# Kernel tuning notes

Measured on AMD Instinct MI355X. Metric: run time of the kernel, lower is better.

## Reference

```python
import jax, jax.numpy as jnp
import numpy as np

NEG_SLOPE = 0.2


def setup_inputs() -> dict:
    key = jax.random.key(0)
    ks = jax.random.split(key, 5)
    N, E, Din, Dout = 100000, 1600000, 64, 64
    x = jax.random.normal(ks[0], (N, Din), dtype=jnp.float32)
    edge_index = jax.random.randint(ks[1], (2, E), 0, N, dtype=jnp.int64)
    # Glorot-ish scale for weights
    W_l = jax.random.normal(ks[2], (Din, Dout), dtype=jnp.float32) / np.sqrt(Din)
    W_r = jax.random.normal(ks[3], (Din, Dout), dtype=jnp.float32) / np.sqrt(Din)
    att = jax.random.normal(ks[4], (Dout,), dtype=jnp.float32) / np.sqrt(Dout)
    bias = jnp.zeros((Dout,), dtype=jnp.float32)
    return {"x": x, "edge_index": edge_index, "W_l": W_l, "W_r": W_r, "att": att, "bias": bias}


def reference(x, edge_index, W_l, W_r, att, bias):
    N = x.shape[0]
    # PyG GATv2Conv default: add self loops
    loop = jnp.arange(N, dtype=edge_index.dtype)
    src = jnp.concatenate([edge_index[0], loop])  # j (source / message)
    dst = jnp.concatenate([edge_index[1], loop])  # i (target / aggregation)

    x_l = x @ W_l  # [N, Dout] source transform
    x_r = x @ W_r  # [N, Dout] target transform

    # per-edge attention logit: att . LeakyReLU(x_l[j] + x_r[i])
    e = jax.nn.leaky_relu(x_l[src] + x_r[dst], NEG_SLOPE) @ att  # [E+N]

    # segment softmax grouped by destination node
    e_max = jax.ops.segment_max(e, dst, num_segments=N)  # [N]
    e_exp = jnp.exp(e - e_max[dst])
    denom = jax.ops.segment_sum(e_exp, dst, num_segments=N)  # [N]
    alpha = e_exp / denom[dst]  # [E+N]

    # weighted scatter-add aggregation of source features
    out = jax.ops.segment_sum(alpha[:, None] * x_l[src], dst, num_segments=N)
    return out + bias
```

## Files before the change

kernel.cpp:

```cpp
#include <hip/hip_runtime.h>

#define NEG_SLOPE 0.2f
#define CH 8192
#define BW 512
#define CAP2 10240

__global__ __launch_bounds__(256) void k_gemm(const float* __restrict__ x,
                                              const float* __restrict__ Wl,
                                              const float* __restrict__ Wr,
                                              float* __restrict__ xl,
                                              float* __restrict__ xr, int N) {
    __shared__ float sX[128 * 64];
    __shared__ float sW[64 * 128];
    const int t = threadIdx.x;
    const int B = blockIdx.x * 128;

    for (int f = t; f < 2048; f += 256) {
        const int k = f >> 5, cg = f & 31;
        float4 v;
        if (cg < 16) v = reinterpret_cast<const float4*>(Wl)[k * 16 + cg];
        else         v = reinterpret_cast<const float4*>(Wr)[k * 16 + (cg - 16)];
        reinterpret_cast<float4*>(sW)[f] = v;
    }
    for (int f = t; f < 2048; f += 256) {
        const int r = B + (f >> 4);
        float4 v = {0.f, 0.f, 0.f, 0.f};
        if (r < N) v = reinterpret_cast<const float4*>(x)[(size_t)B * 16 + f];
        reinterpret_cast<float4*>(sX)[f] = v;
    }
    __syncthreads();

    const int cg = t & 31;
    const int g  = t >> 5;

    float4 acc[16];
#pragma unroll
    for (int i = 0; i < 16; i++) acc[i] = make_float4(0.f, 0.f, 0.f, 0.f);

    for (int kk = 0; kk < 64; kk += 4) {
        const float4 w0 = reinterpret_cast<const float4*>(sW)[(kk + 0) * 32 + cg];
        const float4 w1 = reinterpret_cast<const float4*>(sW)[(kk + 1) * 32 + cg];
        const float4 w2 = reinterpret_cast<const float4*>(sW)[(kk + 2) * 32 + cg];
        const float4 w3 = reinterpret_cast<const float4*>(sW)[(kk + 3) * 32 + cg];
#pragma unroll
        for (int i = 0; i < 16; i++) {
            const float4 xv = reinterpret_cast<const float4*>(sX)[(g * 16 + i) * 16 + (kk >> 2)];
            acc[i].x = fmaf(xv.x, w0.x, acc[i].x);
            acc[i].y = fmaf(xv.x, w0.y, acc[i].y);
            acc[i].z = fmaf(xv.x, w0.z, acc[i].z);
            acc[i].w = fmaf(xv.x, w0.w, acc[i].w);
            acc[i].x = fmaf(xv.y, w1.x, acc[i].x);
            acc[i].y = fmaf(xv.y, w1.y, acc[i].y);
            acc[i].z = fmaf(xv.y, w1.z, acc[i].z);
            acc[i].w = fmaf(xv.y, w1.w, acc[i].w);
            acc[i].x = fmaf(xv.z, w2.x, acc[i].x);
            acc[i].y = fmaf(xv.z, w2.y, acc[i].y);
            acc[i].z = fmaf(xv.z, w2.z, acc[i].z);
            acc[i].w = fmaf(xv.z, w2.w, acc[i].w);
            acc[i].x = fmaf(xv.w, w3.x, acc[i].x);
            acc[i].y = fmaf(xv.w, w3.y, acc[i].y);
            acc[i].z = fmaf(xv.w, w3.z, acc[i].z);
            acc[i].w = fmaf(xv.w, w3.w, acc[i].w);
        }
    }

    const int c = cg * 4;
    float* dstp = (c < 64) ? (xl + c) : (xr + (c - 64));
#pragma unroll
    for (int i = 0; i < 16; i++) {
        const int r = B + g * 16 + i;
        if (r < N) *reinterpret_cast<float4*>(dstp + (size_t)r * 64) = acc[i];
    }
}

__global__ __launch_bounds__(256) void k_part(const int* __restrict__ src,
                                              const int* __restrict__ dst,
                                              int* __restrict__ bcount,
                                              int* __restrict__ part,
                                              int E, int M, int NB) {
    __shared__ int lhist[512];
    __shared__ int lbase[512];
    const int t = threadIdx.x;
    const int b = blockIdx.x;
    const int lo = b * CH, hi = min(M, lo + CH);

    for (int i = t; i < NB; i += 256) lhist[i] = 0;
    __syncthreads();
    for (int k = lo + t; k < hi; k += 256) {
        const int d = (k < E) ? dst[k] : k - E;
        atomicAdd(&lhist[d >> 9], 1);
    }
    __syncthreads();
    for (int i = t; i < NB; i += 256) {
        const int c = lhist[i];
        lbase[i] = c ? atomicAdd(&bcount[i], c) : 0;
    }
    __syncthreads();
    for (int i = t; i < NB; i += 256) lhist[i] = 0;
    __syncthreads();
    for (int k = lo + t; k < hi; k += 256) {
        int s, d;
        if (k < E) { s = src[k]; d = dst[k]; } else { s = k - E; d = s; }
        const int bkt = d >> 9;
        const int pos = lbase[bkt] + atomicAdd(&lhist[bkt], 1);
        if (pos < CAP2) part[(size_t)bkt * CAP2 + pos] = (s << 9) | (d & 511);
    }
}

__global__ __launch_bounds__(256) void k_bsort(const int* __restrict__ part,
                                               const int* __restrict__ bcount,
                                               int* __restrict__ sedge,
                                               int* __restrict__ off,
                                               int* __restrict__ deg, int N) {
    __shared__ int keys[CAP2];
    __shared__ int lhist[512];
    __shared__ int lcur[512];
    __shared__ int sh2[256];
    const int t = threadIdx.x;
    const int bkt = blockIdx.x;
    const int base = bkt * CAP2;
    const int n = min(bcount[bkt], CAP2);

    for (int i = t; i < 512; i += 256) lhist[i] = 0;
    __syncthreads();
    for (int i = t; i < n; i += 256) {
        const int k = part[base + i];
        keys[i] = k;
        atomicAdd(&lhist[k & 511], 1);
    }
    __syncthreads();

    const int a0 = lhist[2 * t], a1 = lhist[2 * t + 1];
    const int ps = a0 + a1;
    sh2[t] = ps;
    __syncthreads();
    for (int o = 1; o < 256; o <<= 1) {
        int v = (t >= o) ? sh2[t - o] : 0;
        __syncthreads();
        sh2[t] += v;
        __syncthreads();
    }
    const int ex = sh2[t] - ps;
    lcur[2 * t]     = base + ex;
    lcur[2 * t + 1] = base + ex + a0;
    const int d0 = (bkt << 9) + 2 * t;
    if (d0 < N)     { off[d0] = base + ex;          deg[d0] = a0; }
    if (d0 + 1 < N) { off[d0 + 1] = base + ex + a0; deg[d0 + 1] = a1; }
    __syncthreads();

    for (int i = t; i < n; i += 256) {
        const int k = keys[i];
        const int pos = atomicAdd(&lcur[k & 511], 1);
        sedge[pos] = k >> 9;
    }
}

__global__ void k_fused(const int* __restrict__ offv, const int* __restrict__ degv,
                        const int* __restrict__ sedge, const float* __restrict__ xl,
                        const float* __restrict__ xr, const float* __restrict__ att,
                        const float* __restrict__ bias, float* __restrict__ out, int N) {
    const int lane = threadIdx.x & 63;
    const int gl = lane & 15;
    const int q = lane >> 4;
    int wave = (blockIdx.x * blockDim.x + threadIdx.x) >> 6;
    const int nw = (gridDim.x * blockDim.x) >> 6;
    const float4 a = reinterpret_cast<const float4*>(att)[gl];
    const float4 b = reinterpret_cast<const float4*>(bias)[gl];
    for (int i = wave; i < N; i += nw) {
        const int base = offv[i];
        const int dg = degv[i];
        const float4 xri = reinterpret_cast<const float4*>(xr)[(size_t)i * 16 + gl];
        float s = 0.f;
        float4 acc = {0.f, 0.f, 0.f, 0.f};
        for (int t = q; t < dg; t += 4) {
            const int j = sedge[base + t];
            const float4 l = reinterpret_cast<const float4*>(xl)[(size_t)j * 16 + gl];
            float v0 = l.x + xri.x; v0 = fmaxf(v0, NEG_SLOPE * v0);
            float v1 = l.y + xri.y; v1 = fmaxf(v1, NEG_SLOPE * v1);
            float v2 = l.z + xri.z; v2 = fmaxf(v2, NEG_SLOPE * v2);
            float v3 = l.w + xri.w; v3 = fmaxf(v3, NEG_SLOPE * v3);
            float p = a.x * v0 + a.y * v1 + a.z * v2 + a.w * v3;
            p += __shfl_xor(p, 1, 16);
            p += __shfl_xor(p, 2, 16);
            p += __shfl_xor(p, 4, 16);
            p += __shfl_xor(p, 8, 16);
            const float w = __expf(p);
            s += w;
            acc.x = fmaf(w, l.x, acc.x);
            acc.y = fmaf(w, l.y, acc.y);
            acc.z = fmaf(w, l.z, acc.z);
            acc.w = fmaf(w, l.w, acc.w);
        }
        s += __shfl_xor(s, 16); s += __shfl_xor(s, 32);
        acc.x += __shfl_xor(acc.x, 16); acc.x += __shfl_xor(acc.x, 32);
        acc.y += __shfl_xor(acc.y, 16); acc.y += __shfl_xor(acc.y, 32);
        acc.z += __shfl_xor(acc.z, 16); acc.z += __shfl_xor(acc.z, 32);
        acc.w += __shfl_xor(acc.w, 16); acc.w += __shfl_xor(acc.w, 32);
        if (q == 0) {
            const float inv = 1.f / s;
            float4 o;
            o.x = fmaf(acc.x, inv, b.x);
            o.y = fmaf(acc.y, inv, b.y);
            o.z = fmaf(acc.z, inv, b.z);
            o.w = fmaf(acc.w, inv, b.w);
            reinterpret_cast<float4*>(out)[(size_t)i * 16 + gl] = o;
        }
    }
}

extern "C" void kernel_launch(void* const* d_in, const int* in_sizes, int n_in,
                              void* d_out, int out_size, void* d_ws, size_t ws_size,
                              hipStream_t stream) {
    const float* x    = (const float*)d_in[0];
    const int*   ei   = (const int*)d_in[1];
    const float* Wl   = (const float*)d_in[2];
    const float* Wr   = (const float*)d_in[3];
    const float* att  = (const float*)d_in[4];
    const float* bias = (const float*)d_in[5];
    float* out = (float*)d_out;

    const int N = in_sizes[0] / 64;
    const int E = in_sizes[1] / 2;
    const int M = E + N;
    const int ng  = (N + 127) / 128;
    const int nch = (M + CH - 1) / CH;
    const int NB  = (N + BW - 1) / BW;

    float* xl = (float*)d_ws;
    float* xr = xl + (size_t)N * 64;
    int* deg    = (int*)(xr + (size_t)N * 64);
    int* off    = deg + N;
    int* bcount = off + N;
    int* part   = bcount + NB;
    int* sedge  = part + (size_t)NB * CAP2;

    hipMemsetAsync(bcount, 0, (size_t)NB * sizeof(int), stream);

    k_gemm<<<ng, 256, 0, stream>>>(x, Wl, Wr, xl, xr, N);
    k_part<<<nch, 256, 0, stream>>>(ei, ei + E, bcount, part, E, M, NB);
    k_bsort<<<NB, 256, 0, stream>>>(part, bcount, sedge, off, deg, N);
    k_fused<<<2048, 256, 0, stream>>>(off, deg, sedge, xl, xr, att, bias, out, N);
}
```

Baseline: 238.9 us.

## Store projected features in fp16 and coalesce partition and sort scatters via LDS

The projected source and target features are now written and gathered as fp16, which halves the bytes moved by the random per-edge gathers in the fused aggregation kernel. The partition kernel now reads its edges into registers, ranks them per bucket in shared memory, and writes them out bucket-contiguously instead of scattering with per-edge atomics. The bucket sort stages its sorted output in LDS before a coalesced store. fp16 storage loses precision in the attention logits and aggregated features, and the larger shared-memory use in the partition and sort kernels may reduce occupancy.

```diff
diff --git a/kernel.cpp b/kernel.cpp
--- a/kernel.cpp
+++ b/kernel.cpp
@@ -1,15 +1,17 @@
 #include <hip/hip_runtime.h>
+#include <hip/hip_fp16.h>
 
 #define NEG_SLOPE 0.2f
-#define CH 8192
+#define CH 4096
+#define UN 16
 #define BW 512
 #define CAP2 10240
 
 __global__ __launch_bounds__(256) void k_gemm(const float* __restrict__ x,
                                               const float* __restrict__ Wl,
                                               const float* __restrict__ Wr,
-                                              float* __restrict__ xl,
-                                              float* __restrict__ xr, int N) {
+                                              __half* __restrict__ xl,
+                                              __half* __restrict__ xr, int N) {
     __shared__ float sX[128 * 64];
     __shared__ float sW[64 * 128];
     const int t = threadIdx.x;
@@ -65,11 +67,21 @@
     }
 
     const int c = cg * 4;
-    float* dstp = (c < 64) ? (xl + c) : (xr + (c - 64));
+    __half* dstp = (c < 64) ? (xl + c) : (xr + (c - 64));
 #pragma unroll
     for (int i = 0; i < 16; i++) {
         const int r = B + g * 16 + i;
-        if (r < N) *reinterpret_cast<float4*>(dstp + (size_t)r * 64) = acc[i];
+        if (r < N) {
+            __half2 h01, h23;
+            h01.x = __float2half_rn(acc[i].x);
+            h01.y = __float2half_rn(acc[i].y);
+            h23.x = __float2half_rn(acc[i].z);
+            h23.y = __float2half_rn(acc[i].w);
+            uint2 u;
+            u.x = *reinterpret_cast<unsigned int*>(&h01);
+            u.y = *reinterpret_cast<unsigned int*>(&h23);
+            *reinterpret_cast<uint2*>(dstp + (size_t)r * 64) = u;
+        }
     }
 }
 
@@ -78,32 +90,66 @@
                                               int* __restrict__ bcount,
                                               int* __restrict__ part,
                                               int E, int M, int NB) {
-    __shared__ int lhist[512];
-    __shared__ int lbase[512];
+    __shared__ int skey[CH];
+    __shared__ unsigned char sbkt[CH];
+    __shared__ int hist[256];
+    __shared__ int lcur[256];
+    __shared__ int gofs[256];
     const int t = threadIdx.x;
     const int b = blockIdx.x;
-    const int lo = b * CH, hi = min(M, lo + CH);
-
-    for (int i = t; i < NB; i += 256) lhist[i] = 0;
-    __syncthreads();
-    for (int k = lo + t; k < hi; k += 256) {
-        const int d = (k < E) ? dst[k] : k - E;
-        atomicAdd(&lhist[d >> 9], 1);
-    }
-    __syncthreads();
-    for (int i = t; i < NB; i += 256) {
-        const int c = lhist[i];
-        lbase[i] = c ? atomicAdd(&bcount[i], c) : 0;
-    }
-    __syncthreads();
-    for (int i = t; i < NB; i += 256) lhist[i] = 0;
-    __syncthreads();
-    for (int k = lo + t; k < hi; k += 256) {
-        int s, d;
-        if (k < E) { s = src[k]; d = dst[k]; } else { s = k - E; d = s; }
-        const int bkt = d >> 9;
-        const int pos = lbase[bkt] + atomicAdd(&lhist[bkt], 1);
-        if (pos < CAP2) part[(size_t)bkt * CAP2 + pos] = (s << 9) | (d & 511);
+    const int lo = b * CH;
+    const int cnt = min(M - lo, CH);
+
+    hist[t] = 0;
+    __syncthreads();
+
+    int rs[UN], rd[UN];
+#pragma unroll
+    for (int u = 0; u < UN; u++) {
+        const int k = lo + t + u * 256;
+        rd[u] = -1; rs[u] = 0;
+        if (k < M) {
+            if (k < E) { rs[u] = src[k]; rd[u] = dst[k]; }
+            else       { rs[u] = k - E;  rd[u] = rs[u]; }
+        }
+    }
+#pragma unroll
+    for (int u = 0; u < UN; u++)
+        if (rd[u] >= 0) atomicAdd(&hist[rd[u] >> 9], 1);
+    __syncthreads();
+
+    const int h = hist[t];
+    lcur[t] = h;
+    __syncthreads();
+    for (int o = 1; o < 256; o <<= 1) {
+        const int v = (t >= o) ? lcur[t - o] : 0;
+        __syncthreads();
+        lcur[t] += v;
+        __syncthreads();
+    }
+    const int ex = lcur[t] - h;
+    int gbase = 0;
+    if (t < NB && h > 0) gbase = atomicAdd(&bcount[t], h);
+    __syncthreads();
+    lcur[t] = ex;
+    gofs[t] = t * CAP2 + gbase - ex;
+    __syncthreads();
+
+#pragma unroll
+    for (int u = 0; u < UN; u++) {
+        if (rd[u] >= 0) {
+            const int bkt = rd[u] >> 9;
+            const int p = atomicAdd(&lcur[bkt], 1);
+            skey[p] = (rs[u] << 9) | (rd[u] & 511);
+            sbkt[p] = (unsigned char)bkt;
+        }
+    }
+    __syncthreads();
+
+    for (int i = t; i < cnt; i += 256) {
+        const int bkt = sbkt[i];
+        const int pos = gofs[bkt] + i;
+        if (pos - bkt * CAP2 < CAP2) part[pos] = skey[i];
     }
 }
 
@@ -113,6 +159,7 @@
                                                int* __restrict__ off,
                                                int* __restrict__ deg, int N) {
     __shared__ int keys[CAP2];
+    __shared__ int outk[CAP2];
     __shared__ int lhist[512];
     __shared__ int lcur[512];
     __shared__ int sh2[256];
@@ -141,8 +188,8 @@
         __syncthreads();
     }
     const int ex = sh2[t] - ps;
-    lcur[2 * t]     = base + ex;
-    lcur[2 * t + 1] = base + ex + a0;
+    lcur[2 * t]     = ex;
+    lcur[2 * t + 1] = ex + a0;
     const int d0 = (bkt << 9) + 2 * t;
     if (d0 < N)     { off[d0] = base + ex;          deg[d0] = a0; }
     if (d0 + 1 < N) { off[d0 + 1] = base + ex + a0; deg[d0 + 1] = a1; }
@@ -151,13 +198,15 @@
     for (int i = t; i < n; i += 256) {
         const int k = keys[i];
         const int pos = atomicAdd(&lcur[k & 511], 1);
-        sedge[pos] = k >> 9;
-    }
+        outk[pos] = k >> 9;
+    }
+    __syncthreads();
+    for (int i = t; i < n; i += 256) sedge[base + i] = outk[i];
 }
 
 __global__ void k_fused(const int* __restrict__ offv, const int* __restrict__ degv,
-                        const int* __restrict__ sedge, const float* __restrict__ xl,
-                        const float* __restrict__ xr, const float* __restrict__ att,
+                        const int* __restrict__ sedge, const __half* __restrict__ xl,
+                        const __half* __restrict__ xr, const float* __restrict__ att,
                         const float* __restrict__ bias, float* __restrict__ out, int N) {
     const int lane = threadIdx.x & 63;
     const int gl = lane & 15;
@@ -169,16 +218,20 @@
     for (int i = wave; i < N; i += nw) {
         const int base = offv[i];
         const int dg = degv[i];
-        const float4 xri = reinterpret_cast<const float4*>(xr)[(size_t)i * 16 + gl];
+        const uint2 xru = reinterpret_cast<const uint2*>(xr + (size_t)i * 64)[gl];
+        const float2 r01 = __half22float2(*reinterpret_cast<const __half2*>(&xru.x));
+        const float2 r23 = __half22float2(*reinterpret_cast<const __half2*>(&xru.y));
         float s = 0.f;
         float4 acc = {0.f, 0.f, 0.f, 0.f};
         for (int t = q; t < dg; t += 4) {
             const int j = sedge[base + t];
-            const float4 l = reinterpret_cast<const float4*>(xl)[(size_t)j * 16 + gl];
-            float v0 = l.x + xri.x; v0 = fmaxf(v0, NEG_SLOPE * v0);
-            float v1 = l.y + xri.y; v1 = fmaxf(v1, NEG_SLOPE * v1);
-            float v2 = l.z + xri.z; v2 = fmaxf(v2, NEG_SLOPE * v2);
-            float v3 = l.w + xri.w; v3 = fmaxf(v3, NEG_SLOPE * v3);
+            const uint2 xu = reinterpret_cast<const uint2*>(xl + (size_t)j * 64)[gl];
+            const float2 l01 = __half22float2(*reinterpret_cast<const __half2*>(&xu.x));
+            const float2 l23 = __half22float2(*reinterpret_cast<const __half2*>(&xu.y));
+            float v0 = l01.x + r01.x; v0 = fmaxf(v0, NEG_SLOPE * v0);
+            float v1 = l01.y + r01.y; v1 = fmaxf(v1, NEG_SLOPE * v1);
+            float v2 = l23.x + r23.x; v2 = fmaxf(v2, NEG_SLOPE * v2);
+            float v3 = l23.y + r23.y; v3 = fmaxf(v3, NEG_SLOPE * v3);
             float p = a.x * v0 + a.y * v1 + a.z * v2 + a.w * v3;
             p += __shfl_xor(p, 1, 16);
             p += __shfl_xor(p, 2, 16);
@@ -186,10 +239,10 @@
             p += __shfl_xor(p, 8, 16);
             const float w = __expf(p);
             s += w;
-            acc.x = fmaf(w, l.x, acc.x);
-            acc.y = fmaf(w, l.y, acc.y);
-            acc.z = fmaf(w, l.z, acc.z);
-            acc.w = fmaf(w, l.w, acc.w);
+            acc.x = fmaf(w, l01.x, acc.x);
+            acc.y = fmaf(w, l01.y, acc.y);
+            acc.z = fmaf(w, l23.x, acc.z);
+            acc.w = fmaf(w, l23.y, acc.w);
         }
         s += __shfl_xor(s, 16); s += __shfl_xor(s, 32);
         acc.x += __shfl_xor(acc.x, 16); acc.x += __shfl_xor(acc.x, 32);
@@ -226,8 +279,8 @@
     const int nch = (M + CH - 1) / CH;
     const int NB  = (N + BW - 1) / BW;
 
-    float* xl = (float*)d_ws;
-    float* xr = xl + (size_t)N * 64;
+    __half* xl = (__half*)d_ws;
+    __half* xr = xl + (size_t)N * 64;
     int* deg    = (int*)(xr + (size_t)N * 64);
     int* off    = deg + N;
     int* bcount = off + N;
```

New measurement: 216.9 us. -9.2%, faster.
